# Kernel optimization log

Measured on AMD Instinct MI355X. Metric: run time of the kernel, lower is better.

The kernel has to match this reference:

```python
import jax, jax.numpy as jnp
import numpy as np

B, I, D, H, DP = 2, 256, 768, 12, 128
DK = D // H  # 64
NPQ, NPV = 4, 8  # query/key points and value points per head


def setup_inputs() -> dict:
    key = jax.random.key(0)
    ks = jax.random.split(key, 24)
    s = 0.02
    w = lambda k, shp: (jax.random.normal(k, shp, jnp.float32) * s)
    inp = {
        "x1d": jax.random.normal(ks[0], (B, I, D), jnp.float32),
        "x2d": jax.random.normal(ks[1], (B, I, I, DP), jnp.float32),
        "past_T": jax.random.normal(ks[2], (B, I, 3), jnp.float32),
        "past_R": jax.random.normal(ks[3], (B, I, 3, 3), jnp.float32),
        "last_T": jax.random.normal(ks[4], (B, I, 3), jnp.float32),
        "last_R": jax.random.normal(ks[5], (B, I, 3, 3), jnp.float32),
        "bias": jax.random.normal(ks[6], (B, H, I, I), jnp.float32) * 0.1,
        "Wq": w(ks[7], (D, D)),
        "Wk": w(ks[8], (D, D)),
        "Wv": w(ks[9], (D, D)),
        "W_pair_bias": w(ks[10], (DP, H)),
        "Wpq_past": w(ks[11], (D, H * NPQ * 3)),
        "Wpk_past": w(ks[12], (D, H * NPQ * 3)),
        "Wpv_past": w(ks[13], (D, H * NPV * 3)),
        "Wpq_last": w(ks[14], (D, H * NPQ * 3)),
        "Wpk_last": w(ks[15], (D, H * NPQ * 3)),
        "Wpv_last": w(ks[16], (D, H * NPV * 3)),
        "tpw_past": jax.random.uniform(ks[17], (H,), jnp.float32),
        "tpw_last": jax.random.uniform(ks[18], (H,), jnp.float32),
        "W_pair_value": w(ks[19], (DP, D)),
        "W_out": w(ks[20], (2 * D + 2 * H * 8 * 4, D)),
        "b_out": jnp.zeros((D,), jnp.float32),
    }
    return inp


def reference(x1d, x2d, past_T, past_R, last_T, last_R, bias,
              Wq, Wk, Wv, W_pair_bias,
              Wpq_past, Wpk_past, Wpv_past,
              Wpq_last, Wpk_last, Wpv_last,
              tpw_past, tpw_last, W_pair_value, W_out, b_out):
    b, i, d = x1d.shape
    h = tpw_past.shape[0]
    dk = d // h
    scalar_w = 1.0 / np.sqrt(3.0 * dk)
    point_w = 1.0 / np.sqrt(3.0 * 4.0 * 9.0 / 2.0)
    pair_w = 1.0 / np.sqrt(3.0)

    # scalar attention
    q = (x1d @ Wq).reshape(b, i, h, dk)
    k = (x1d @ Wk).reshape(b, i, h, dk)
    v = (x1d @ Wv).reshape(b, i, h, dk)
    scalar_attn = jnp.einsum('bihc,bjhc->bhij', q * scalar_w, k)

    past_IR = jnp.swapaxes(past_R, -1, -2)
    last_IR = jnp.swapaxes(last_R, -1, -2)

    def affine(pts, T, IR):  # pts: [b,i,h,c,3]
        return jnp.einsum('bipq,bihcq->bihcp', IR, pts) + T[:, :, None, None, :]

    def point_branch(Wpq, Wpk, Wpv, T, IR, tpw):
        qp = (x1d @ Wpq).reshape(b, i, h, NPQ, 3)
        kp = (x1d @ Wpk).reshape(b, i, h, NPQ, 3)
        vp = (x1d @ Wpv).reshape(b, i, h, NPV, 3)
        qg, kg, vg = affine(qp, T, IR), affine(kp, T, IR), affine(vp, T, IR)
        # pairwise point distances: [b,i,j,h,NPQ]
        dist = jnp.linalg.norm(qg[:, :, None] - kg[:, None], axis=-1)
        pw = point_w * jax.nn.softplus(tpw)  # [h]
        attn = -0.5 * pw[:, None, None] * jnp.transpose(dist.sum(-1), (0, 3, 1, 2))
        return attn, vg

    pa_past, vg_past = point_branch(Wpq_past, Wpk_past, Wpv_past, past_T, past_IR, tpw_past)
    pa_last, vg_last = point_branch(Wpq_last, Wpk_last, Wpv_last, last_T, last_IR, tpw_last)

    pair_attn = pair_w * jnp.transpose(x2d @ W_pair_bias, (0, 3, 1, 2))  # bhij

    attn = jax.nn.softmax(scalar_attn + pa_past + pa_last + pair_attn + bias, axis=-1)

    out_scalar = jnp.einsum('bhij,bjhc->bihc', attn, v).reshape(b, i, d)
    og_past = jnp.einsum('bhij,bjhcp->bihcp', attn, vg_past)
    og_last = jnp.einsum('bhij,bjhcp->bihcp', attn, vg_last)

    # NOTE: the original module inverts BOTH branches with the PAST pose (faithful).
    def inv_past(og):
        return jnp.einsum('bipq,bihcq->bihcp', past_R, og - past_T[:, :, None, None, :])

    ol_past = inv_past(og_past)
    ol_last = inv_past(og_last)
    n_past = jnp.linalg.norm(ol_past, axis=-1).reshape(b, i, h * NPV)
    n_last = jnp.linalg.norm(ol_last, axis=-1).reshape(b, i, h * NPV)
    ol_past = ol_past.reshape(b, i, h * NPV * 3)
    ol_last = ol_last.reshape(b, i, h * NPV * 3)

    v_pair = (x2d @ W_pair_value).reshape(b, i, i, h, dk)
    out_pair = jnp.einsum('bhij,bijhc->bihc', attn, v_pair).reshape(b, i, d)

    feat = jnp.concatenate([out_pair, out_scalar, ol_past, n_past, ol_last, n_last], axis=-1)
    return feat @ W_out + b_out  # dropout is identity at eval
```

## Files before the change

### kernel.cpp

```cpp
#include <hip/hip_runtime.h>
#include <hip/hip_bf16.h>
#include <math.h>

#define BB 2
#define II 256
#define DD 768
#define HH 12
#define DPP 128
#define NPQ 4
#define NPV 8
#define FEAT_DIM 2304
#define NPACK 3456

#define OFF_QKVPTS ((size_t)0)
#define OFF_PBATTN ((size_t)1769472)
#define OFF_X1DB   ((size_t)3342336)
#define OFF_VT     OFF_X1DB
#define OFF_W1T    ((size_t)3538944)
#define OFF_ABF    OFF_W1T
#define OFF_W2T    ((size_t)4866048)
#define OFF_FEATB  ((size_t)5750784)
#define OFF_QPTS   ((size_t)6340608)
#define OFF_KPTS   ((size_t)6488064)
#define OFF_QKHM   ((size_t)6635520)
#define OFF_VGJT   ((size_t)7028736)
#define OFF_WPVT   ((size_t)7176192)

#define SCALAR_W 0.07216878364870323f
#define POINT_W  0.13608276348795434f
#define PAIR_W   0.57735026918962576f

typedef __attribute__((ext_vector_type(8))) short short8;
typedef __attribute__((ext_vector_type(4))) short short4v;
typedef __attribute__((ext_vector_type(4))) float f32x4;

__device__ inline ushort f2bf(float f) {
  __hip_bfloat16 h = __float2bfloat16(f);
  return *reinterpret_cast<ushort*>(&h);
}
__device__ inline float bf2f(short u) {
  return __uint_as_float(((unsigned int)(unsigned short)u) << 16);
}

struct TJob { const float* src; ushort* dst; int K, N, sStride, dStride, nx, ny; };
struct TJobs { TJob j[11]; };

__global__ __launch_bounds__(256)
void prep_kernel(const float* __restrict__ x2d, const float* __restrict__ Wpb,
                 const float* __restrict__ bias, ushort* __restrict__ pbattn,
                 const float* __restrict__ x1d, ushort* __restrict__ x1db,
                 TJobs jobs) {
  __shared__ __align__(16) char smem[9216];
  const int blk = blockIdx.x;
  const int tid = threadIdx.x;
  if (blk < 1024) {
    ushort* wpbT_s = (ushort*)smem;
    ushort* pb_s   = (ushort*)(smem + 4352);
    const int bi = blk >> 1, half = blk & 1;
    const int b = bi >> 8, i = bi & 255;
    for (int u = tid; u < 2048; u += 256) {
      const int h = u >> 7, p = u & 127;
      wpbT_s[h * 136 + p] = (h < 12) ? f2bf(Wpb[p * 12 + h]) : (ushort)0;
    }
    __syncthreads();
    const int lane = tid & 63, w = tid >> 6;
    const int l15 = lane & 15, kq = lane >> 4;
    const float* xbase = x2d + ((size_t)bi * II + half * 128) * DPP;
#pragma unroll
    for (int mi = 0; mi < 2; ++mi) {
      const int mt = w + mi * 4;
      const int jl = mt * 16 + l15;
      const float* arow = xbase + (size_t)jl * DPP;
      f32x4 acc = {};
#pragma unroll
      for (int kk = 0; kk < 4; ++kk) {
        const float4 f0 = *reinterpret_cast<const float4*>(arow + kk * 32 + kq * 8);
        const float4 f1 = *reinterpret_cast<const float4*>(arow + kk * 32 + kq * 8 + 4);
        short8 af;
        af[0] = (short)f2bf(f0.x); af[1] = (short)f2bf(f0.y);
        af[2] = (short)f2bf(f0.z); af[3] = (short)f2bf(f0.w);
        af[4] = (short)f2bf(f1.x); af[5] = (short)f2bf(f1.y);
        af[6] = (short)f2bf(f1.z); af[7] = (short)f2bf(f1.w);
        const short8 bf = *reinterpret_cast<const short8*>(&wpbT_s[l15 * 136 + kk * 32 + kq * 8]);
        acc = __builtin_amdgcn_mfma_f32_16x16x32_bf16(af, bf, acc, 0, 0, 0);
      }
#pragma unroll
      for (int rr = 0; rr < 4; ++rr)
        pb_s[(mt * 16 + kq * 4 + rr) * 18 + l15] = f2bf(acc[rr]);
    }
    __syncthreads();
    if (tid < 192) {
      const int h = tid >> 4, jq = tid & 15;
      const int jl0 = jq * 8;
      const size_t base = (((size_t)(b * HH + h) * II + i) * II) + half * 128 + jl0;
      const float4 bv0 = *reinterpret_cast<const float4*>(bias + base);
      const float4 bv1 = *reinterpret_cast<const float4*>(bias + base + 4);
      const float bv[8] = {bv0.x, bv0.y, bv0.z, bv0.w, bv1.x, bv1.y, bv1.z, bv1.w};
      short8 o;
#pragma unroll
      for (int e = 0; e < 8; ++e)
        o[e] = (short)f2bf(PAIR_W * bf2f((short)pb_s[(jl0 + e) * 18 + h]) + bv[e]);
      *reinterpret_cast<short8*>(pbattn + base) = o;
    }
  } else if (blk < 1216) {
    const int idx = (blk - 1024) * 256 + tid;
    if (idx < 512 * 768 / 8) {
      const float4 f0 = reinterpret_cast<const float4*>(x1d)[idx * 2 + 0];
      const float4 f1 = reinterpret_cast<const float4*>(x1d)[idx * 2 + 1];
      short8 v;
      v[0] = (short)f2bf(f0.x); v[1] = (short)f2bf(f0.y);
      v[2] = (short)f2bf(f0.z); v[3] = (short)f2bf(f0.w);
      v[4] = (short)f2bf(f1.x); v[5] = (short)f2bf(f1.y);
      v[6] = (short)f2bf(f1.z); v[7] = (short)f2bf(f1.w);
      reinterpret_cast<short8*>(x1db)[idx] = v;
    }
  } else {
    float (*t)[33] = (float(*)[33])smem;
    int blk2 = blk - 1216;
#pragma unroll 1
    for (int jj = 0; jj < 11; ++jj) {
      const TJob J = jobs.j[jj];
      const int cnt = J.nx * J.ny;
      if (blk2 < cnt) {
        const int n0 = (blk2 % J.nx) * 32, k0 = (blk2 / J.nx) * 32;
        const int c = tid & 31, r = tid >> 5;
#pragma unroll
        for (int u = 0; u < 4; ++u) {
          const int kk = r + u * 8;
          t[kk][c] = (n0 + c < J.N) ? J.src[(size_t)(k0 + kk) * J.sStride + n0 + c] : 0.f;
        }
        __syncthreads();
#pragma unroll
        for (int u = 0; u < 4; ++u) {
          const int n = n0 + r + u * 8;
          if (n < J.N) J.dst[(size_t)n * J.dStride + k0 + c] = f2bf(t[c][r + u * 8]);
        }
        return;
      }
      blk2 -= cnt;
    }
  }
}

__global__ __launch_bounds__(256)
void mfma_gemm_kernel(const ushort* __restrict__ A, const ushort* __restrict__ Bt,
                      float* __restrict__ C, const float* __restrict__ bias,
                      ushort* __restrict__ Cb, ushort* __restrict__ Vt, int N, int K) {
  __shared__ short a_s[64 * 64];
  __shared__ short b_s[64 * 64];
  const int tid = threadIdx.x;
  const int lane = tid & 63;
  const int wave = tid >> 6;
  const int wm = wave >> 1, wn = wave & 1;
  const int m0 = blockIdx.x * 64, n0 = blockIdx.y * 64;
  const int lrow = tid >> 3, lch = tid & 7;
  const int l15 = lane & 15, l7 = lane & 7, kq = lane >> 4;
  f32x4 acc[2][2] = {};
  for (int kc = 0; kc < K; kc += 64) {
#pragma unroll
    for (int u = 0; u < 2; ++u) {
      const int r = lrow + u * 32;
      const short8 av = *reinterpret_cast<const short8*>(A  + (size_t)(m0 + r) * K + kc + lch * 8);
      const short8 bv = *reinterpret_cast<const short8*>(Bt + (size_t)(n0 + r) * K + kc + lch * 8);
      const int sc = ((lch ^ (r & 7)) << 3);
      *reinterpret_cast<short8*>(&a_s[r * 64 + sc]) = av;
      *reinterpret_cast<short8*>(&b_s[r * 64 + sc]) = bv;
    }
    __syncthreads();
#pragma unroll
    for (int kk = 0; kk < 64; kk += 32) {
      const int ch = (kk >> 3) + kq;
      const int cx = ((ch ^ l7) << 3);
      short8 af[2], bf[2];
      af[0] = *reinterpret_cast<const short8*>(&a_s[(wm * 32 +      l15) * 64 + cx]);
      af[1] = *reinterpret_cast<const short8*>(&a_s[(wm * 32 + 16 + l15) * 64 + cx]);
      bf[0] = *reinterpret_cast<const short8*>(&b_s[(wn * 32 +      l15) * 64 + cx]);
      bf[1] = *reinterpret_cast<const short8*>(&b_s[(wn * 32 + 16 + l15) * 64 + cx]);
#pragma unroll
      for (int mt = 0; mt < 2; ++mt)
#pragma unroll
        for (int nt = 0; nt < 2; ++nt)
          acc[mt][nt] = __builtin_amdgcn_mfma_f32_16x16x32_bf16(af[mt], bf[nt], acc[mt][nt], 0, 0, 0);
    }
    __syncthreads();
  }
#pragma unroll
  for (int mt = 0; mt < 2; ++mt) {
    const int r0 = m0 + wm * 32 + mt * 16 + kq * 4;
#pragma unroll
    for (int nt = 0; nt < 2; ++nt) {
      const int c = n0 + wn * 32 + nt * 16 + l15;
      const float bv = bias ? bias[c] : 0.f;
#pragma unroll
      for (int rr = 0; rr < 4; ++rr) {
        const float val = acc[mt][nt][rr] + bv;
        const int m = r0 + rr;
        if (!Cb) {
          C[(size_t)m * N + c] = val;
        } else if (c < 1536) {
          const int bb = m >> 8, ii = m & 255;
          const int plane = (c >= 768) ? 1 : 0;
          const int hh = (c & 767) >> 6, cc2 = c & 63;
          Cb[((((size_t)plane * BB + bb) * HH + hh) * II + ii) * 64 + cc2] = f2bf(val);
        } else if (c < 2304) {
          const int bb = m >> 8, ii = m & 255;
          Vt[((size_t)bb * DD + (c - 1536)) * II + ii] = f2bf(val);
        } else {
          C[(size_t)m * N + c] = val;
        }
      }
    }
  }
}

struct XfJob { const float* T; const float* R; float* dstf; ushort* dstb;
               int np; int sub; int srccol; int mode; };
struct XfJobs { XfJob j[6]; };

__global__ __launch_bounds__(256)
void transform_kernel(const float* __restrict__ qkvpts, XfJobs jobs) {
  const XfJob J = jobs.j[blockIdx.y];
  const int idx = blockIdx.x * 256 + threadIdx.x;
  if (J.mode == 1) {
    const int hn = HH * J.np;
    if (idx >= BB * II * hn) return;
    const int bi = idx / hn, rem = idx - bi * hn;
    const float* p = qkvpts + (size_t)bi * NPACK + J.srccol + rem * 3;
    const float p0 = p[0], p1 = p[1], p2 = p[2];
    const float* R = J.R + (size_t)bi * 9;
    const float* T = J.T + (size_t)bi * 3;
    const float o0 = R[0] * p0 + R[3] * p1 + R[6] * p2 + T[0];
    const float o1 = R[1] * p0 + R[4] * p1 + R[7] * p2 + T[1];
    const float o2 = R[2] * p0 + R[5] * p1 + R[8] * p2 + T[2];
    const int h = rem / J.np, n = rem - h * J.np;
    const int b = bi >> 8, i = bi & 255;
    float* d = J.dstf + ((size_t)(b * HH + h) * II + i) * 24 + J.sub + n * 3;
    d[0] = o0; d[1] = o1; d[2] = o2;
  } else {
    if (idx >= BB * HH * J.np * II) return;
    const int i = idx & 255;
    int r2 = idx >> 8;
    const int n = r2 % J.np; r2 /= J.np;
    const int h = r2 % HH;
    const int b = r2 / HH;
    const int bi = b * II + i;
    const float* p = qkvpts + (size_t)bi * NPACK + J.srccol + (h * J.np + n) * 3;
    const float p0 = p[0], p1 = p[1], p2 = p[2];
    const float* R = J.R + (size_t)bi * 9;
    const float* T = J.T + (size_t)bi * 3;
    const float o0 = R[0] * p0 + R[3] * p1 + R[6] * p2 + T[0];
    const float o1 = R[1] * p0 + R[4] * p1 + R[7] * p2 + T[1];
    const float o2 = R[2] * p0 + R[5] * p1 + R[8] * p2 + T[2];
    if (J.mode == 2) {
      const int col = J.sub + h * 24 + n * 3;
      ushort* d = J.dstb + ((size_t)b * 576 + col) * II + i;
      d[0] = f2bf(o0); d[II] = f2bf(o1); d[2 * II] = f2bf(o2);
    } else {
      float* d = J.dstf + ((size_t)(b * HH + h) * 24 + J.sub + n * 3) * II + i;
      d[0] = o0; d[II] = o1; d[2 * II] = o2;
    }
  }
}

__global__ __launch_bounds__(256)
void attn_kernel(const ushort* __restrict__ qkhm,
                 const float* __restrict__ qpts, const float* __restrict__ kpts,
                 const float* __restrict__ tpw_past, const float* __restrict__ tpw_last,
                 const ushort* __restrict__ pbattn, ushort* __restrict__ abf) {
  __shared__ float qp_s[16 * 24];
  __shared__ float pb_s[16 * 260];
  __shared__ float red_s[2][16 * 4];
  __shared__ ushort a_lds[16 * 264];
  const int tid = threadIdx.x;
  const int lane = tid & 63;
  const int w = tid >> 6;
  const int i0 = blockIdx.x * 16;
  const int h = blockIdx.y;
  const int b = blockIdx.z;
  const size_t bh = (size_t)b * HH + h;
  if (tid < 96)
    reinterpret_cast<float4*>(qp_s)[tid] =
        reinterpret_cast<const float4*>(qpts + (bh * II + i0) * 24)[tid];
  {
    const ushort* src = pbattn + (bh * II + i0) * II;
    for (int u = tid; u < 512; u += 256) {
      const int r = u >> 5, c8 = u & 31;
      const short8 v = *reinterpret_cast<const short8*>(src + (size_t)r * II + c8 * 8);
      float* d = &pb_s[r * 260 + c8 * 8];
#pragma unroll
      for (int e = 0; e < 8; ++e) d[e] = bf2f(v[e]);
    }
  }
  __syncthreads();
  const int l15 = lane & 15, kq = lane >> 4;
  const ushort* qrow = qkhm + (((size_t)b * HH + h) * II + i0 + l15) * 64;
  const ushort* kplane = qkhm + (((size_t)(BB + b) * HH + h) * II) * 64;
  const short8 af0 = *reinterpret_cast<const short8*>(qrow + kq * 8);
  const short8 af1 = *reinterpret_cast<const short8*>(qrow + 32 + kq * 8);
  const float pwp = 0.5f * POINT_W * log1pf(expf(tpw_past[h]));
  const float pwl = 0.5f * POINT_W * log1pf(expf(tpw_last[h]));
  const float* kpt = kpts + bh * 6144;
  float lg[4][4];
#pragma unroll
  for (int jb = 0; jb < 4; ++jb) {
    const int j = w * 64 + jb * 16 + l15;
    const ushort* krow = kplane + (size_t)j * 64;
    f32x4 acc = {};
    acc = __builtin_amdgcn_mfma_f32_16x16x32_bf16(
        af0, *reinterpret_cast<const short8*>(krow + kq * 8), acc, 0, 0, 0);
    acc = __builtin_amdgcn_mfma_f32_16x16x32_bf16(
        af1, *reinterpret_cast<const short8*>(krow + 32 + kq * 8), acc, 0, 0, 0);
    float kg[24];
#pragma unroll
    for (int c = 0; c < 24; ++c) kg[c] = kpt[c * 256 + j];
#pragma unroll
    for (int rr = 0; rr < 4; ++rr) {
      const int il = kq * 4 + rr;
      const float* qg = &qp_s[il * 24];
      float dp = 0.f, dl = 0.f;
#pragma unroll
      for (int n = 0; n < 4; ++n) {
        float dx = qg[n * 3] - kg[n * 3], dy = qg[n * 3 + 1] - kg[n * 3 + 1],
              dz = qg[n * 3 + 2] - kg[n * 3 + 2];
        dp += sqrtf(dx * dx + dy * dy + dz * dz);
        dx = qg[12 + n * 3] - kg[12 + n * 3]; dy = qg[12 + n * 3 + 1] - kg[12 + n * 3 + 1];
        dz = qg[12 + n * 3 + 2] - kg[12 + n * 3 + 2];
        dl += sqrtf(dx * dx + dy * dy + dz * dz);
      }
      lg[jb][rr] = SCALAR_W * acc[rr] - pwp * dp - pwl * dl + pb_s[il * 260 + j];
    }
  }
#pragma unroll
  for (int rr = 0; rr < 4; ++rr) {
    float m = fmaxf(fmaxf(lg[0][rr], lg[1][rr]), fmaxf(lg[2][rr], lg[3][rr]));
    m = fmaxf(m, __shfl_xor(m, 1));
    m = fmaxf(m, __shfl_xor(m, 2));
    m = fmaxf(m, __shfl_xor(m, 4));
    m = fmaxf(m, __shfl_xor(m, 8));
    if (l15 == 0) red_s[0][(kq * 4 + rr) * 4 + w] = m;
  }
  __syncthreads();
#pragma unroll
  for (int rr = 0; rr < 4; ++rr) {
    const int il = kq * 4 + rr;
    const float* r = &red_s[0][il * 4];
    const float m = fmaxf(fmaxf(r[0], r[1]), fmaxf(r[2], r[3]));
    float s = 0.f;
#pragma unroll
    for (int jb = 0; jb < 4; ++jb) { lg[jb][rr] = __expf(lg[jb][rr] - m); s += lg[jb][rr]; }
    s += __shfl_xor(s, 1); s += __shfl_xor(s, 2);
    s += __shfl_xor(s, 4); s += __shfl_xor(s, 8);
    if (l15 == 0) red_s[1][il * 4 + w] = s;
  }
  __syncthreads();
#pragma unroll
  for (int rr = 0; rr < 4; ++rr) {
    const int il = kq * 4 + rr;
    const float* r = &red_s[1][il * 4];
    const float inv = 1.f / (r[0] + r[1] + r[2] + r[3]);
#pragma unroll
    for (int jb = 0; jb < 4; ++jb)
      a_lds[il * 264 + w * 64 + jb * 16 + l15] = f2bf(lg[jb][rr] * inv);
  }
  __syncthreads();
  ushort* ab = abf + (bh * II + i0) * II;
#pragma unroll
  for (int u = 0; u < 2; ++u) {
    const int idx = tid + u * 256;
    const int r = idx >> 5, cc = idx & 31;
    *reinterpret_cast<short8*>(ab + (size_t)r * II + cc * 8) =
        *reinterpret_cast<const short8*>(&a_lds[r * 264 + cc * 8]);
  }
}

__global__ __launch_bounds__(256)
void wpair_av_kernel(const float* __restrict__ x2d, const ushort* __restrict__ abf,
                     const ushort* __restrict__ wpvt,
                     const ushort* __restrict__ vt, const ushort* __restrict__ vgjt,
                     const float* __restrict__ past_T, const float* __restrict__ past_R,
                     ushort* __restrict__ featb) {
  __shared__ __align__(16) char smem[33792];
  const int blk = blockIdx.x;
  const int tid = threadIdx.x;
  const int lane = tid & 63, w = tid >> 6;
  const int l15 = lane & 15, kq = lane >> 4;
  if (blk < 512) {
    ushort* a_s = (ushort*)smem;
    ushort* tb  = (ushort*)(smem + 8192);
    float*  t_s = (float*)(smem + 25600);
    const int bi = blk;
    const int b = bi >> 8, i = bi & 255;
#pragma unroll
    for (int u = 0; u < 2; ++u) {
      const int c = tid + u * 256;
      const int h = c >> 5, ch = c & 31;
      short8 v = {};
      if (h < 12)
        v = *reinterpret_cast<const short8*>(abf + (((size_t)(b * HH + h) * II + i) * II) + ch * 8);
      *reinterpret_cast<short8*>(&a_s[h * 256 + ((ch ^ h) << 3)]) = v;
    }
    const int n0 = w * 32;
    f32x4 acc[2] = {};
    for (int jt = 0; jt < 4; ++jt) {
      __syncthreads();
      const float4* src = reinterpret_cast<const float4*>(x2d + ((size_t)bi * II + jt * 64) * DPP);
#pragma unroll
      for (int u = 0; u < 8; ++u) {
        const int fid = tid + u * 256;
        const int j = fid >> 5, p4 = (fid & 31) * 4;
        const float4 v = src[fid];
        short4v o;
        o[0] = (short)f2bf(v.x); o[1] = (short)f2bf(v.y);
        o[2] = (short)f2bf(v.z); o[3] = (short)f2bf(v.w);
        *reinterpret_cast<short4v*>(&tb[j * 136 + (p4 ^ ((j >> 3) << 4))]) = o;
      }
      __syncthreads();
#pragma unroll
      for (int nt = 0; nt < 2; ++nt) {
        const int p = n0 + nt * 16 + l15;
#pragma unroll
        for (int kk = 0; kk < 2; ++kk) {
          const int ch32 = jt * 8 + kk * 4 + kq;
          const short8 af = *reinterpret_cast<const short8*>(&a_s[l15 * 256 + ((ch32 ^ l15) << 3)]);
          short8 bf;
#pragma unroll
          for (int e = 0; e < 8; ++e) {
            const int row = kk * 32 + kq * 8 + e;
            bf[e] = (short)tb[row * 136 + (p ^ ((row >> 3) << 4))];
          }
          acc[nt] = __builtin_amdgcn_mfma_f32_16x16x32_bf16(af, bf, acc[nt], 0, 0, 0);
        }
      }
    }
#pragma unroll
    for (int nt = 0; nt < 2; ++nt) {
      const int p = n0 + nt * 16 + l15;
#pragma unroll
      for (int r = 0; r < 4; ++r) t_s[(kq * 4 + r) * 128 + p] = acc[nt][r];
    }
    __syncthreads();
    ushort* fout = featb + (size_t)bi * FEAT_DIM;
#pragma unroll
    for (int u = 0; u < 3; ++u) {
      const int c = tid + u * 256;
      const int h = c >> 6;
      const ushort* wr = wpvt + (size_t)c * DPP;
      float o = 0.f;
      for (int p = 0; p < DPP; p += 8) {
        const short8 wv = *reinterpret_cast<const short8*>(wr + p);
#pragma unroll
        for (int e = 0; e < 8; ++e) o += t_s[h * 128 + p + e] * bf2f(wv[e]);
      }
      fout[c] = f2bf(o);
    }
  } else {
    ushort* a_s = (ushort*)smem;
    float*  c_s = (float*)(smem + 16384);
    const int blk2 = blk - 512;
    const int it = blk2 & 7;
    const int rest = blk2 >> 3;
    const int h = rest % 12;
    const int b = rest / 12;
    const int i0 = it * 32;
    const size_t bh = (size_t)b * HH + h;
    {
      const ushort* src = abf + (bh * II + i0) * II;
#pragma unroll
      for (int u = 0; u < 4; ++u) {
        const int cidx = tid + u * 256;
        const int r = cidx >> 5, ch = cidx & 31;
        const short8 v = *reinterpret_cast<const short8*>(src + (size_t)r * II + ch * 8);
        *reinterpret_cast<short8*>(&a_s[r * 256 + ((ch ^ (r & 7)) << 3)]) = v;
      }
    }
    __syncthreads();
    for (int t = w; t < 14; t += 4) {
      const int mt = t / 7, nt = t % 7;
      const int c = nt * 16 + l15;
      const ushort* bcol;
      if (c < 64)      bcol = vt   + ((size_t)b * DD + h * 64 + c) * II;
      else if (c < 88) bcol = vgjt + ((size_t)b * 576 + h * 24 + (c - 64)) * II;
      else             bcol = vgjt + ((size_t)b * 576 + 288 + h * 24 + (c - 88)) * II;
      f32x4 acc = {};
#pragma unroll
      for (int ks = 0; ks < 8; ++ks) {
        const int ch = ks * 4 + kq;
        const int r = mt * 16 + l15;
        const short8 af = *reinterpret_cast<const short8*>(&a_s[r * 256 + ((ch ^ (r & 7)) << 3)]);
        const short8 bf = *reinterpret_cast<const short8*>(bcol + ks * 32 + kq * 8);
        acc = __builtin_amdgcn_mfma_f32_16x16x32_bf16(af, bf, acc, 0, 0, 0);
      }
#pragma unroll
      for (int rr = 0; rr < 4; ++rr) c_s[(mt * 16 + kq * 4 + rr) * 116 + c] = acc[rr];
    }
    __syncthreads();
    {
      const int il = tid >> 3, c0 = (tid & 7) * 8;
      ushort* fo = featb + (size_t)(b * II + i0 + il) * FEAT_DIM + 768 + h * 64 + c0;
      short8 o;
#pragma unroll
      for (int e = 0; e < 8; ++e) o[e] = (short)f2bf(c_s[il * 116 + c0 + e]);
      *reinterpret_cast<short8*>(fo) = o;
    }
    for (int u = tid; u < 512; u += 256) {
      const int il = u >> 4;
      const int br = (u >> 3) & 1;
      const int n = u & 7;
      const int bi = b * II + i0 + il;
      const float* T = past_T + (size_t)bi * 3;
      const float* R = past_R + (size_t)bi * 9;
      const int cb = 64 + br * 24 + n * 3;
      const float o0 = c_s[il * 116 + cb + 0] - T[0];
      const float o1 = c_s[il * 116 + cb + 1] - T[1];
      const float o2 = c_s[il * 116 + cb + 2] - T[2];
      const float l0 = R[0] * o0 + R[1] * o1 + R[2] * o2;
      const float l1 = R[3] * o0 + R[4] * o1 + R[5] * o2;
      const float l2 = R[6] * o0 + R[7] * o1 + R[8] * o2;
      const float nn = sqrtf(l0 * l0 + l1 * l1 + l2 * l2);
      const int r = h * 8 + n;
      ushort* fout = featb + (size_t)bi * FEAT_DIM;
      const int olbase = br ? 1920 : 1536;
      const int nbase  = br ? 2208 : 1824;
      fout[olbase + r * 3 + 0] = f2bf(l0);
      fout[olbase + r * 3 + 1] = f2bf(l1);
      fout[olbase + r * 3 + 2] = f2bf(l2);
      fout[nbase + r] = f2bf(nn);
    }
  }
}

extern "C" void kernel_launch(void* const* d_in, const int* in_sizes, int n_in,
                              void* d_out, int out_size, void* d_ws, size_t ws_size,
                              hipStream_t stream) {
  (void)in_sizes; (void)n_in; (void)out_size; (void)ws_size;
  const float* x1d      = (const float*)d_in[0];
  const float* x2d      = (const float*)d_in[1];
  const float* past_T   = (const float*)d_in[2];
  const float* past_R   = (const float*)d_in[3];
  const float* last_T   = (const float*)d_in[4];
  const float* last_R   = (const float*)d_in[5];
  const float* bias     = (const float*)d_in[6];
  const float* Wq       = (const float*)d_in[7];
  const float* Wk       = (const float*)d_in[8];
  const float* Wv       = (const float*)d_in[9];
  const float* Wpb      = (const float*)d_in[10];
  const float* Wpq_past = (const float*)d_in[11];
  const float* Wpk_past = (const float*)d_in[12];
  const float* Wpv_past = (const float*)d_in[13];
  const float* Wpq_last = (const float*)d_in[14];
  const float* Wpk_last = (const float*)d_in[15];
  const float* Wpv_last = (const float*)d_in[16];
  const float* tpw_past = (const float*)d_in[17];
  const float* tpw_last = (const float*)d_in[18];
  const float* W_pair_value = (const float*)d_in[19];
  const float* W_out    = (const float*)d_in[20];
  const float* b_out    = (const float*)d_in[21];
  float* out = (float*)d_out;
  float* ws  = (float*)d_ws;

  float*  qkvpts = ws + OFF_QKVPTS;
  ushort* pbattn = (ushort*)(ws + OFF_PBATTN);
  ushort* x1db   = (ushort*)(ws + OFF_X1DB);
  ushort* vt     = (ushort*)(ws + OFF_VT);
  ushort* w1t    = (ushort*)(ws + OFF_W1T);
  ushort* abf    = (ushort*)(ws + OFF_ABF);
  ushort* w2t    = (ushort*)(ws + OFF_W2T);
  ushort* featb  = (ushort*)(ws + OFF_FEATB);
  float*  qpts   = ws + OFF_QPTS;
  float*  kpts   = ws + OFF_KPTS;
  ushort* qkhm   = (ushort*)(ws + OFF_QKHM);
  ushort* vgjt   = (ushort*)(ws + OFF_VGJT);
  ushort* wpvt   = (ushort*)(ws + OFF_WPVT);

  const dim3 blk256(256);

  {
    TJobs jobs = {};
    jobs.j[0]  = {Wq,       w1t + (size_t)   0 * 768, DD,      DD,   DD,  768,  24, 24};
    jobs.j[1]  = {Wk,       w1t + (size_t) 768 * 768, DD,      DD,   DD,  768,  24, 24};
    jobs.j[2]  = {Wv,       w1t + (size_t)1536 * 768, DD,      DD,   DD,  768,  24, 24};
    jobs.j[3]  = {Wpq_past, w1t + (size_t)2304 * 768, DD,     144,   144, 768,   5, 24};
    jobs.j[4]  = {Wpk_past, w1t + (size_t)2448 * 768, DD,     144,   144, 768,   5, 24};
    jobs.j[5]  = {Wpv_past, w1t + (size_t)2592 * 768, DD,     288,   288, 768,   9, 24};
    jobs.j[6]  = {Wpq_last, w1t + (size_t)2880 * 768, DD,     144,   144, 768,   5, 24};
    jobs.j[7]  = {Wpk_last, w1t + (size_t)3024 * 768, DD,     144,   144, 768,   5, 24};
    jobs.j[8]  = {Wpv_last, w1t + (size_t)3168 * 768, DD,     288,   288, 768,   9, 24};
    jobs.j[9]  = {W_out,    w2t,                      FEAT_DIM, DD,  DD,  2304, 24, 72};
    jobs.j[10] = {W_pair_value, wpvt,                 DPP,     DD,   DD,  DPP,  24,  4};
    int tblocks = 0;
    for (int j = 0; j < 11; ++j) tblocks += jobs.j[j].nx * jobs.j[j].ny;
    prep_kernel<<<dim3(1216 + tblocks), blk256, 0, stream>>>(
        x2d, Wpb, bias, pbattn, x1d, x1db, jobs);
  }

  mfma_gemm_kernel<<<dim3(8, 54), blk256, 0, stream>>>(
      x1db, w1t, qkvpts, nullptr, qkhm, vt, NPACK, DD);

  {
    XfJobs jobs = {};
    jobs.j[0] = {past_T, past_R, qpts, nullptr, NPQ,   0, 2304, 1};
    jobs.j[1] = {past_T, past_R, kpts, nullptr, NPQ,   0, 2448, 3};
    jobs.j[2] = {past_T, past_R, nullptr, vgjt, NPV,   0, 2592, 2};
    jobs.j[3] = {last_T, last_R, qpts, nullptr, NPQ,  12, 2880, 1};
    jobs.j[4] = {last_T, last_R, kpts, nullptr, NPQ,  12, 3024, 3};
    jobs.j[5] = {last_T, last_R, nullptr, vgjt, NPV, 288, 3168, 2};
    transform_kernel<<<dim3(192, 6), blk256, 0, stream>>>(qkvpts, jobs);
  }

  attn_kernel<<<dim3(16, HH, BB), blk256, 0, stream>>>(
      qkhm, qpts, kpts, tpw_past, tpw_last, pbattn, abf);

  wpair_av_kernel<<<dim3(704), blk256, 0, stream>>>(
      x2d, abf, wpvt, vt, vgjt, past_T, past_R, featb);

  mfma_gemm_kernel<<<dim3(8, 12), blk256, 0, stream>>>(
      featb, w2t, out, b_out, nullptr, nullptr, DD, FEAT_DIM);
}
```

Before: 115.3 us.

## Fuse attention-value products into attention kernel and split pair-bias prep finer

The attention kernel now also computes the attn·V, attn·Vg products and the inverse-pose transform straight from its LDS-resident probabilities. This drops the separate AV blocks, which had to reload the probability matrix from global memory. The remaining pair-value projection becomes its own kernel that runs afterwards. The pair-bias part of the prep kernel now uses quarter-row blocks instead of half-row blocks, giving more, smaller blocks. The probability LDS tile uses an XOR swizzle to avoid bank conflicts during the MFMA operand reads.

```diff
diff --git a/kernel.cpp b/kernel.cpp
--- a/kernel.cpp
+++ b/kernel.cpp
@@ -53,10 +53,10 @@
   __shared__ __align__(16) char smem[9216];
   const int blk = blockIdx.x;
   const int tid = threadIdx.x;
-  if (blk < 1024) {
+  if (blk < 2048) {
     ushort* wpbT_s = (ushort*)smem;
     ushort* pb_s   = (ushort*)(smem + 4352);
-    const int bi = blk >> 1, half = blk & 1;
+    const int bi = blk >> 2, quarter = blk & 3;
     const int b = bi >> 8, i = bi & 255;
     for (int u = tid; u < 2048; u += 256) {
       const int h = u >> 7, p = u & 127;
@@ -65,11 +65,9 @@
     __syncthreads();
     const int lane = tid & 63, w = tid >> 6;
     const int l15 = lane & 15, kq = lane >> 4;
-    const float* xbase = x2d + ((size_t)bi * II + half * 128) * DPP;
-#pragma unroll
-    for (int mi = 0; mi < 2; ++mi) {
-      const int mt = w + mi * 4;
-      const int jl = mt * 16 + l15;
+    const float* xbase = x2d + ((size_t)bi * II + quarter * 64) * DPP;
+    {
+      const int jl = w * 16 + l15;
       const float* arow = xbase + (size_t)jl * DPP;
       f32x4 acc = {};
 #pragma unroll
@@ -86,13 +84,13 @@
       }
 #pragma unroll
       for (int rr = 0; rr < 4; ++rr)
-        pb_s[(mt * 16 + kq * 4 + rr) * 18 + l15] = f2bf(acc[rr]);
+        pb_s[(w * 16 + kq * 4 + rr) * 18 + l15] = f2bf(acc[rr]);
     }
     __syncthreads();
-    if (tid < 192) {
-      const int h = tid >> 4, jq = tid & 15;
+    if (tid < 96) {
+      const int h = tid >> 3, jq = tid & 7;
       const int jl0 = jq * 8;
-      const size_t base = (((size_t)(b * HH + h) * II + i) * II) + half * 128 + jl0;
+      const size_t base = (((size_t)(b * HH + h) * II + i) * II) + quarter * 64 + jl0;
       const float4 bv0 = *reinterpret_cast<const float4*>(bias + base);
       const float4 bv1 = *reinterpret_cast<const float4*>(bias + base + 4);
       const float bv[8] = {bv0.x, bv0.y, bv0.z, bv0.w, bv1.x, bv1.y, bv1.z, bv1.w};
@@ -102,8 +100,8 @@
         o[e] = (short)f2bf(PAIR_W * bf2f((short)pb_s[(jl0 + e) * 18 + h]) + bv[e]);
       *reinterpret_cast<short8*>(pbattn + base) = o;
     }
-  } else if (blk < 1216) {
-    const int idx = (blk - 1024) * 256 + tid;
+  } else if (blk < 2240) {
+    const int idx = (blk - 2048) * 256 + tid;
     if (idx < 512 * 768 / 8) {
       const float4 f0 = reinterpret_cast<const float4*>(x1d)[idx * 2 + 0];
       const float4 f1 = reinterpret_cast<const float4*>(x1d)[idx * 2 + 1];
@@ -116,7 +114,7 @@
     }
   } else {
     float (*t)[33] = (float(*)[33])smem;
-    int blk2 = blk - 1216;
+    int blk2 = blk - 2240;
 #pragma unroll 1
     for (int jj = 0; jj < 11; ++jj) {
       const TJob J = jobs.j[jj];
@@ -263,14 +261,17 @@
 }
 
 __global__ __launch_bounds__(256)
-void attn_kernel(const ushort* __restrict__ qkhm,
-                 const float* __restrict__ qpts, const float* __restrict__ kpts,
-                 const float* __restrict__ tpw_past, const float* __restrict__ tpw_last,
-                 const ushort* __restrict__ pbattn, ushort* __restrict__ abf) {
+void attn_av_kernel(const ushort* __restrict__ qkhm,
+                    const float* __restrict__ qpts, const float* __restrict__ kpts,
+                    const float* __restrict__ tpw_past, const float* __restrict__ tpw_last,
+                    const ushort* __restrict__ pbattn, ushort* __restrict__ abf,
+                    const ushort* __restrict__ vt, const ushort* __restrict__ vgjt,
+                    const float* __restrict__ past_T, const float* __restrict__ past_R,
+                    ushort* __restrict__ featb) {
   __shared__ float qp_s[16 * 24];
   __shared__ float pb_s[16 * 260];
   __shared__ float red_s[2][16 * 4];
-  __shared__ ushort a_lds[16 * 264];
+  __shared__ ushort a_lds[16 * 256];
   const int tid = threadIdx.x;
   const int lane = tid & 63;
   const int w = tid >> 6;
@@ -359,8 +360,11 @@
     const float* r = &red_s[1][il * 4];
     const float inv = 1.f / (r[0] + r[1] + r[2] + r[3]);
 #pragma unroll
-    for (int jb = 0; jb < 4; ++jb)
-      a_lds[il * 264 + w * 64 + jb * 16 + l15] = f2bf(lg[jb][rr] * inv);
+    for (int jb = 0; jb < 4; ++jb) {
+      const int j = w * 64 + jb * 16 + l15;
+      const int ch = j >> 3;
+      a_lds[il * 256 + ((ch ^ (il & 7)) << 3) + (j & 7)] = f2bf(lg[jb][rr] * inv);
+    }
   }
   __syncthreads();
   ushort* ab = abf + (bh * II + i0) * II;
@@ -369,140 +373,38 @@
     const int idx = tid + u * 256;
     const int r = idx >> 5, cc = idx & 31;
     *reinterpret_cast<short8*>(ab + (size_t)r * II + cc * 8) =
-        *reinterpret_cast<const short8*>(&a_lds[r * 264 + cc * 8]);
-  }
-}
-
-__global__ __launch_bounds__(256)
-void wpair_av_kernel(const float* __restrict__ x2d, const ushort* __restrict__ abf,
-                     const ushort* __restrict__ wpvt,
-                     const ushort* __restrict__ vt, const ushort* __restrict__ vgjt,
-                     const float* __restrict__ past_T, const float* __restrict__ past_R,
-                     ushort* __restrict__ featb) {
-  __shared__ __align__(16) char smem[33792];
-  const int blk = blockIdx.x;
-  const int tid = threadIdx.x;
-  const int lane = tid & 63, w = tid >> 6;
-  const int l15 = lane & 15, kq = lane >> 4;
-  if (blk < 512) {
-    ushort* a_s = (ushort*)smem;
-    ushort* tb  = (ushort*)(smem + 8192);
-    float*  t_s = (float*)(smem + 25600);
-    const int bi = blk;
-    const int b = bi >> 8, i = bi & 255;
-#pragma unroll
-    for (int u = 0; u < 2; ++u) {
-      const int c = tid + u * 256;
-      const int h = c >> 5, ch = c & 31;
-      short8 v = {};
-      if (h < 12)
-        v = *reinterpret_cast<const short8*>(abf + (((size_t)(b * HH + h) * II + i) * II) + ch * 8);
-      *reinterpret_cast<short8*>(&a_s[h * 256 + ((ch ^ h) << 3)]) = v;
-    }
-    const int n0 = w * 32;
-    f32x4 acc[2] = {};
-    for (int jt = 0; jt < 4; ++jt) {
-      __syncthreads();
-      const float4* src = reinterpret_cast<const float4*>(x2d + ((size_t)bi * II + jt * 64) * DPP);
-#pragma unroll
-      for (int u = 0; u < 8; ++u) {
-        const int fid = tid + u * 256;
-        const int j = fid >> 5, p4 = (fid & 31) * 4;
-        const float4 v = src[fid];
-        short4v o;
-        o[0] = (short)f2bf(v.x); o[1] = (short)f2bf(v.y);
-        o[2] = (short)f2bf(v.z); o[3] = (short)f2bf(v.w);
-        *reinterpret_cast<short4v*>(&tb[j * 136 + (p4 ^ ((j >> 3) << 4))]) = o;
-      }
-      __syncthreads();
-#pragma unroll
-      for (int nt = 0; nt < 2; ++nt) {
-        const int p = n0 + nt * 16 + l15;
-#pragma unroll
-        for (int kk = 0; kk < 2; ++kk) {
-          const int ch32 = jt * 8 + kk * 4 + kq;
-          const short8 af = *reinterpret_cast<const short8*>(&a_s[l15 * 256 + ((ch32 ^ l15) << 3)]);
-          short8 bf;
-#pragma unroll
-          for (int e = 0; e < 8; ++e) {
-            const int row = kk * 32 + kq * 8 + e;
-            bf[e] = (short)tb[row * 136 + (p ^ ((row >> 3) << 4))];
-          }
-          acc[nt] = __builtin_amdgcn_mfma_f32_16x16x32_bf16(af, bf, acc[nt], 0, 0, 0);
-        }
-      }
-    }
-#pragma unroll
-    for (int nt = 0; nt < 2; ++nt) {
-      const int p = n0 + nt * 16 + l15;
-#pragma unroll
-      for (int r = 0; r < 4; ++r) t_s[(kq * 4 + r) * 128 + p] = acc[nt][r];
-    }
-    __syncthreads();
-    ushort* fout = featb + (size_t)bi * FEAT_DIM;
-#pragma unroll
-    for (int u = 0; u < 3; ++u) {
-      const int c = tid + u * 256;
-      const int h = c >> 6;
-      const ushort* wr = wpvt + (size_t)c * DPP;
-      float o = 0.f;
-      for (int p = 0; p < DPP; p += 8) {
-        const short8 wv = *reinterpret_cast<const short8*>(wr + p);
-#pragma unroll
-        for (int e = 0; e < 8; ++e) o += t_s[h * 128 + p + e] * bf2f(wv[e]);
-      }
-      fout[c] = f2bf(o);
-    }
-  } else {
-    ushort* a_s = (ushort*)smem;
-    float*  c_s = (float*)(smem + 16384);
-    const int blk2 = blk - 512;
-    const int it = blk2 & 7;
-    const int rest = blk2 >> 3;
-    const int h = rest % 12;
-    const int b = rest / 12;
-    const int i0 = it * 32;
-    const size_t bh = (size_t)b * HH + h;
-    {
-      const ushort* src = abf + (bh * II + i0) * II;
-#pragma unroll
-      for (int u = 0; u < 4; ++u) {
-        const int cidx = tid + u * 256;
-        const int r = cidx >> 5, ch = cidx & 31;
-        const short8 v = *reinterpret_cast<const short8*>(src + (size_t)r * II + ch * 8);
-        *reinterpret_cast<short8*>(&a_s[r * 256 + ((ch ^ (r & 7)) << 3)]) = v;
-      }
-    }
-    __syncthreads();
-    for (int t = w; t < 14; t += 4) {
-      const int mt = t / 7, nt = t % 7;
-      const int c = nt * 16 + l15;
-      const ushort* bcol;
-      if (c < 64)      bcol = vt   + ((size_t)b * DD + h * 64 + c) * II;
-      else if (c < 88) bcol = vgjt + ((size_t)b * 576 + h * 24 + (c - 64)) * II;
-      else             bcol = vgjt + ((size_t)b * 576 + 288 + h * 24 + (c - 88)) * II;
-      f32x4 acc = {};
-#pragma unroll
-      for (int ks = 0; ks < 8; ++ks) {
-        const int ch = ks * 4 + kq;
-        const int r = mt * 16 + l15;
-        const short8 af = *reinterpret_cast<const short8*>(&a_s[r * 256 + ((ch ^ (r & 7)) << 3)]);
-        const short8 bf = *reinterpret_cast<const short8*>(bcol + ks * 32 + kq * 8);
-        acc = __builtin_amdgcn_mfma_f32_16x16x32_bf16(af, bf, acc, 0, 0, 0);
-      }
-#pragma unroll
-      for (int rr = 0; rr < 4; ++rr) c_s[(mt * 16 + kq * 4 + rr) * 116 + c] = acc[rr];
-    }
-    __syncthreads();
-    {
-      const int il = tid >> 3, c0 = (tid & 7) * 8;
-      ushort* fo = featb + (size_t)(b * II + i0 + il) * FEAT_DIM + 768 + h * 64 + c0;
-      short8 o;
-#pragma unroll
-      for (int e = 0; e < 8; ++e) o[e] = (short)f2bf(c_s[il * 116 + c0 + e]);
-      *reinterpret_cast<short8*>(fo) = o;
-    }
-    for (int u = tid; u < 512; u += 256) {
+        *reinterpret_cast<const short8*>(&a_lds[r * 256 + ((cc ^ (r & 7)) << 3)]);
+  }
+  float* c_s = pb_s;
+  for (int t = w; t < 7; t += 4) {
+    const int c = t * 16 + l15;
+    const ushort* bcol;
+    if (c < 64)      bcol = vt   + ((size_t)b * DD + h * 64 + c) * II;
+    else if (c < 88) bcol = vgjt + ((size_t)b * 576 + h * 24 + (c - 64)) * II;
+    else             bcol = vgjt + ((size_t)b * 576 + 288 + h * 24 + (c - 88)) * II;
+    f32x4 acc = {};
+#pragma unroll
+    for (int ks = 0; ks < 8; ++ks) {
+      const int ch = ks * 4 + kq;
+      const short8 af = *reinterpret_cast<const short8*>(&a_lds[l15 * 256 + ((ch ^ (l15 & 7)) << 3)]);
+      const short8 bf = *reinterpret_cast<const short8*>(bcol + ks * 32 + kq * 8);
+      acc = __builtin_amdgcn_mfma_f32_16x16x32_bf16(af, bf, acc, 0, 0, 0);
+    }
+#pragma unroll
+    for (int rr = 0; rr < 4; ++rr) c_s[(kq * 4 + rr) * 120 + c] = acc[rr];
+  }
+  __syncthreads();
+  if (tid < 128) {
+    const int il = tid >> 3, c0 = (tid & 7) * 8;
+    ushort* fo = featb + (size_t)(b * II + i0 + il) * FEAT_DIM + 768 + h * 64 + c0;
+    short8 o;
+#pragma unroll
+    for (int e = 0; e < 8; ++e) o[e] = (short)f2bf(c_s[il * 120 + c0 + e]);
+    *reinterpret_cast<short8*>(fo) = o;
+  }
+  {
+    const int u = tid;
+    if (u < 256) {
       const int il = u >> 4;
       const int br = (u >> 3) & 1;
       const int n = u & 7;
@@ -510,9 +412,9 @@
       const float* T = past_T + (size_t)bi * 3;
       const float* R = past_R + (size_t)bi * 9;
       const int cb = 64 + br * 24 + n * 3;
-      const float o0 = c_s[il * 116 + cb + 0] - T[0];
-      const float o1 = c_s[il * 116 + cb + 1] - T[1];
-      const float o2 = c_s[il * 116 + cb + 2] - T[2];
+      const float o0 = c_s[il * 120 + cb + 0] - T[0];
+      const float o1 = c_s[il * 120 + cb + 1] - T[1];
+      const float o2 = c_s[il * 120 + cb + 2] - T[2];
       const float l0 = R[0] * o0 + R[1] * o1 + R[2] * o2;
       const float l1 = R[3] * o0 + R[4] * o1 + R[5] * o2;
       const float l2 = R[6] * o0 + R[7] * o1 + R[8] * o2;
@@ -526,6 +428,82 @@
       fout[olbase + r * 3 + 2] = f2bf(l2);
       fout[nbase + r] = f2bf(nn);
     }
+  }
+}
+
+__global__ __launch_bounds__(256)
+void wpair_kernel(const float* __restrict__ x2d, const ushort* __restrict__ abf,
+                  const ushort* __restrict__ wpvt, ushort* __restrict__ featb) {
+  __shared__ ushort a_s[16 * 256];
+  __shared__ ushort tb[64 * 136];
+  __shared__ float t_s[16][128];
+  const int tid = threadIdx.x;
+  const int bi = blockIdx.x;
+  const int b = bi >> 8, i = bi & 255;
+#pragma unroll
+  for (int u = 0; u < 2; ++u) {
+    const int c = tid + u * 256;
+    const int h = c >> 5, ch = c & 31;
+    short8 v = {};
+    if (h < 12)
+      v = *reinterpret_cast<const short8*>(abf + (((size_t)(b * HH + h) * II + i) * II) + ch * 8);
+    *reinterpret_cast<short8*>(&a_s[h * 256 + ((ch ^ h) << 3)]) = v;
+  }
+  const int lane = tid & 63, w = tid >> 6;
+  const int l15 = lane & 15, kq = lane >> 4;
+  const int n0 = w * 32;
+  f32x4 acc[2] = {};
+  for (int jt = 0; jt < 4; ++jt) {
+    __syncthreads();
+    const float4* src = reinterpret_cast<const float4*>(x2d + ((size_t)bi * II + jt * 64) * DPP);
+#pragma unroll
+    for (int u = 0; u < 8; ++u) {
+      const int fid = tid + u * 256;
+      const int j = fid >> 5, p4 = (fid & 31) * 4;
+      const float4 v = src[fid];
+      short4v o;
+      o[0] = (short)f2bf(v.x); o[1] = (short)f2bf(v.y);
+      o[2] = (short)f2bf(v.z); o[3] = (short)f2bf(v.w);
+      *reinterpret_cast<short4v*>(&tb[j * 136 + (p4 ^ ((j >> 3) << 4))]) = o;
+    }
+    __syncthreads();
+#pragma unroll
+    for (int nt = 0; nt < 2; ++nt) {
+      const int p = n0 + nt * 16 + l15;
+#pragma unroll
+      for (int kk = 0; kk < 2; ++kk) {
+        const int ch32 = jt * 8 + kk * 4 + kq;
+        const short8 af = *reinterpret_cast<const short8*>(&a_s[l15 * 256 + ((ch32 ^ l15) << 3)]);
+        short8 bf;
+#pragma unroll
+        for (int e = 0; e < 8; ++e) {
+          const int row = kk * 32 + kq * 8 + e;
+          bf[e] = (short)tb[row * 136 + (p ^ ((row >> 3) << 4))];
+        }
+        acc[nt] = __builtin_amdgcn_mfma_f32_16x16x32_bf16(af, bf, acc[nt], 0, 0, 0);
+      }
+    }
+  }
+#pragma unroll
+  for (int nt = 0; nt < 2; ++nt) {
+    const int p = n0 + nt * 16 + l15;
+#pragma unroll
+    for (int r = 0; r < 4; ++r) t_s[kq * 4 + r][p] = acc[nt][r];
+  }
+  __syncthreads();
+  ushort* fout = featb + (size_t)bi * FEAT_DIM;
+#pragma unroll
+  for (int u = 0; u < 3; ++u) {
+    const int c = tid + u * 256;
+    const int h = c >> 6;
+    const ushort* wr = wpvt + (size_t)c * DPP;
+    float o = 0.f;
+    for (int p = 0; p < DPP; p += 8) {
+      const short8 wv = *reinterpret_cast<const short8*>(wr + p);
+#pragma unroll
+      for (int e = 0; e < 8; ++e) o += t_s[h][p + e] * bf2f(wv[e]);
+    }
+    fout[c] = f2bf(o);
   }
 }
 
@@ -589,7 +567,7 @@
     jobs.j[10] = {W_pair_value, wpvt,                 DPP,     DD,   DD,  DPP,  24,  4};
     int tblocks = 0;
     for (int j = 0; j < 11; ++j) tblocks += jobs.j[j].nx * jobs.j[j].ny;
-    prep_kernel<<<dim3(1216 + tblocks), blk256, 0, stream>>>(
+    prep_kernel<<<dim3(2240 + tblocks), blk256, 0, stream>>>(
         x2d, Wpb, bias, pbattn, x1d, x1db, jobs);
   }
 
@@ -607,11 +585,11 @@
     transform_kernel<<<dim3(192, 6), blk256, 0, stream>>>(qkvpts, jobs);
   }
 
-  attn_kernel<<<dim3(16, HH, BB), blk256, 0, stream>>>(
-      qkhm, qpts, kpts, tpw_past, tpw_last, pbattn, abf);
-
-  wpair_av_kernel<<<dim3(704), blk256, 0, stream>>>(
-      x2d, abf, wpvt, vt, vgjt, past_T, past_R, featb);
+  attn_av_kernel<<<dim3(16, HH, BB), blk256, 0, stream>>>(
+      qkhm, qpts, kpts, tpw_past, tpw_last, pbattn, abf,
+      vt, vgjt, past_T, past_R, featb);
+
+  wpair_kernel<<<dim3(BB * II), blk256, 0, stream>>>(x2d, abf, wpvt, featb);
 
   mfma_gemm_kernel<<<dim3(8, 12), blk256, 0, stream>>>(
       featb, w2t, out, b_out, nullptr, nullptr, DD, FEAT_DIM);
```

Result: no change. 116.9 us (+1.4%).
